# Optimization experiments

Measured on AMD Instinct MI355X. Metric: run time of the kernel, lower is better.

## Reference

```python
import jax, jax.numpy as jnp
import numpy as np

K_EDE = 10.0   # self.k
T_EDE = 0.1    # self.t
BN_EPS = 1e-5
T_A = 576.0    # 3*3*64, hardcoded in my_bn1/my_bn2


def qfn(x, prec):
    # dorefa-style round quantizer with straight-through gradient
    n = float(2 ** prec - 1)
    return x + jax.lax.stop_gradient(jnp.round(x * n) / n - x)


@jax.custom_vjp
def binary_quantize(x):
    return jnp.sign(x)


def _bq_fwd(x):
    return jnp.sign(x), x


def _bq_bwd(x, g):
    # IR-Net EDE backward: k * t * (1 - tanh(x*t)^2)
    return (K_EDE * T_EDE * (1.0 - jnp.tanh(x * T_EDE) ** 2) * g,)


binary_quantize.defvjp(_bq_fwd, _bq_bwd)


def _clip_T(x):
    T = jnp.maximum(jnp.abs(x.min()), jnp.abs(x.max()))
    return jax.lax.stop_gradient(jnp.clip(T, 1e-10, 255.0))


def quantize_conv_act(x, prec):
    # my_quantize_conv: clamp to [-T, T], scale to [-1,1], qfn (no rescale by T)
    T = _clip_T(x)
    return qfn(jnp.clip(x, -T, T) / T, prec)


def quantize(x, prec):
    # my_quantize: same but rescaled back by T
    T = _clip_T(x)
    return qfn(jnp.clip(x, -T, T) / T, prec) * T


def ir_conv2d(a, w, stride):
    # IR-Net 1w8a IRConv2d: per-out-channel normalize, binarize (sign), power-of-2 scale
    co = w.shape[0]
    wf = w.reshape(co, -1)
    bw = (w - wf.mean(1)[:, None, None, None]) / jnp.std(wf, axis=1, ddof=1)[:, None, None, None]
    sw = jax.lax.stop_gradient(
        2.0 ** jnp.round(jnp.log2(jnp.abs(bw.reshape(co, -1)).mean(1)))
    )[:, None, None, None]
    bw = binary_quantize(bw) * sw
    return jax.lax.conv_general_dilated(
        a, bw, window_strides=(stride, stride), padding=[(1, 1), (1, 1)],
        dimension_numbers=('NCHW', 'OIHW', 'NCHW'))


def bn_as_quantized_affine(x, gamma, beta, mean, var):
    # my_bn1/my_bn2 (eval mode): BN folded into per-channel scale+bias.
    # The original builds a CxC diagonal 1x1 conv; since off-diagonal entries are 0,
    # both the quantization stats (max|.|) and the conv reduce exactly to this
    # per-channel affine, which is the faithful fused form.
    std = jnp.sqrt(var + BN_EPS)
    w = gamma / std
    b = beta - w * mean
    qw = quantize(w, 3)
    qb = quantize(b, 12)
    aq = qfn(x / T_A, 10) * T_A  # my_quantize_activation(input, 10, T_a)
    return aq * qw[None, :, None, None] + qb[None, :, None, None]


def _block(x, w1, w2, g1, b1, m1, v1, g2, b2, m2, v2):
    xq = quantize_conv_act(x, 3)
    out = ir_conv2d(xq, w1, 1)
    out = bn_as_quantized_affine(out, g1, b1, m1, v1) + xq  # identity shortcut
    out = jnp.clip(out, -1.0, 1.0)  # hardtanh
    x1 = quantize_conv_act(out, 3)
    out = ir_conv2d(x1, w2, 1)
    out = bn_as_quantized_affine(out, g2, b2, m2, v2) + x1
    return jnp.clip(out, -1.0, 1.0)


def setup_inputs() -> dict:
    key = jax.random.key(0)
    ks = jax.random.split(key, 11)
    B, C, H, W = 128, 64, 56, 56
    return {
        'x': jax.random.normal(ks[0], (B, C, H, W), jnp.float32),
        'w1': jax.random.normal(ks[1], (C, C, 3, 3), jnp.float32) * 0.1,
        'w2': jax.random.normal(ks[2], (C, C, 3, 3), jnp.float32) * 0.1,
        'g1': jax.random.uniform(ks[3], (C,), jnp.float32, 0.5, 1.5),
        'b1': jax.random.normal(ks[4], (C,), jnp.float32) * 0.1,
        'm1': jax.random.normal(ks[5], (C,), jnp.float32) * 0.1,
        'v1': jax.random.uniform(ks[6], (C,), jnp.float32, 0.5, 1.5),
        'g2': jax.random.uniform(ks[7], (C,), jnp.float32, 0.5, 1.5),
        'b2': jax.random.normal(ks[8], (C,), jnp.float32) * 0.1,
        'm2': jax.random.normal(ks[9], (C,), jnp.float32) * 0.1,
        'v2': jax.random.uniform(ks[10], (C,), jnp.float32, 0.5, 1.5),
    }


def reference(x, w1, w2, g1, b1, m1, v1, g2, b2, m2, v2):
    return _block(x, w1, w2, g1, b1, m1, v1, g2, b2, m2, v2)
```

## Files before the change

### kernel.cpp

```cpp
#include <hip/hip_runtime.h>
#include <stdint.h>

typedef int v4i   __attribute__((ext_vector_type(4)));
typedef int v16i  __attribute__((ext_vector_type(16)));

#define B_    128
#define C_    64
#define H_    56
#define W_    56
#define HW_   3136
#define NELEM (B_*C_*HW_)

#define OFF_K0   0
#define OFF_K1   ((size_t)NELEM)
#define OFF_WB   ((size_t)2*NELEM)
#define OFF_PAR  (OFF_WB + 2*9*64*64)
#define OFF_MAX  (OFF_PAR + 384*4)

__global__ void k_absmax(const float* __restrict__ x, unsigned* __restrict__ maxbits) {
    __shared__ float smax[4];
    float m = 0.f;
    const int n4 = NELEM / 4;
    for (int i = blockIdx.x * blockDim.x + threadIdx.x; i < n4; i += gridDim.x * blockDim.x) {
        float4 v = ((const float4*)x)[i];
        m = fmaxf(m, fmaxf(fmaxf(fabsf(v.x), fabsf(v.y)), fmaxf(fabsf(v.z), fabsf(v.w))));
    }
    for (int off = 32; off; off >>= 1) m = fmaxf(m, __shfl_down(m, off, 64));
    if ((threadIdx.x & 63) == 0) smax[threadIdx.x >> 6] = m;
    __syncthreads();
    if (threadIdx.x == 0) {
        float mm = fmaxf(fmaxf(smax[0], smax[1]), fmaxf(smax[2], smax[3]));
        atomicMax(maxbits, __float_as_uint(mm));
    }
}

__global__ void k_quant(const float* __restrict__ x, const unsigned* __restrict__ maxbits,
                        int8_t* __restrict__ k8) {
    __shared__ __align__(16) int8_t tile[W_ * C_];
    const int n = blockIdx.x / H_;
    const int y = blockIdx.x % H_;
    const float T = fminf(fmaxf(__uint_as_float(*maxbits), 1e-10f), 255.0f);
    for (int i = threadIdx.x; i < C_ * 14; i += blockDim.x) {
        int c = i / 14, j = i % 14;
        float4 v = *(const float4*)(x + ((size_t)(n * C_ + c)) * HW_ + y * W_ + j * 4);
        float vv[4] = {v.x, v.y, v.z, v.w};
#pragma unroll
        for (int q = 0; q < 4; q++) {
            float t = fminf(fmaxf(vv[q], -T), T);
            float u = __fdiv_rn(t, T);
            int k = (int)rintf(__fmul_rn(u, 7.0f));
            tile[(j * 4 + q) * C_ + c] = (int8_t)k;
        }
    }
    __syncthreads();
    int4* dst = (int4*)(k8 + ((size_t)(n * H_ + y)) * W_ * C_);
    for (int i = threadIdx.x; i < W_ * C_ / 16; i += blockDim.x)
        dst[i] = ((const int4*)tile)[i];
}

__device__ __forceinline__ float pw_reduce64(float r) {
    r = __fadd_rn(r, __shfl_xor(r, 1, 64));
    r = __fadd_rn(r, __shfl_xor(r, 2, 64));
    r = __fadd_rn(r, __shfl_xor(r, 4, 64));
    r = __fadd_rn(r, __shfl_xor(r, 8, 64));
    r = __fadd_rn(r, __shfl_xor(r, 16, 64));
    r = __fadd_rn(r, __shfl_xor(r, 32, 64));
    return r;
}

__global__ void k_prepw(const float* __restrict__ w1, const float* __restrict__ w2,
                        int8_t* __restrict__ wb, float* __restrict__ par) {
    const int layer = blockIdx.x >> 6;
    const int co    = blockIdx.x & 63;
    const float* w = (layer ? w2 : w1) + (size_t)co * 576;
    const int lane = threadIdx.x;
    const int base = (lane >> 3) * 72 + (lane & 7);

    float v[9];
#pragma unroll
    for (int i = 0; i < 9; i++) v[i] = w[base + 8 * i];

    float s = v[0];
#pragma unroll
    for (int i = 1; i < 9; i++) s = __fadd_rn(s, v[i]);
    const float mean = __fdiv_rn(pw_reduce64(s), 576.0f);

    float d0 = __fsub_rn(v[0], mean);
    float sq = __fmul_rn(d0, d0);
#pragma unroll
    for (int i = 1; i < 9; i++) {
        float d = __fsub_rn(v[i], mean);
        sq = __fadd_rn(sq, __fmul_rn(d, d));
    }
    const float sig = __fsqrt_rn(__fdiv_rn(pw_reduce64(sq), 575.0f));

    float sa = fabsf(__fdiv_rn(__fsub_rn(v[0], mean), sig));
#pragma unroll
    for (int i = 1; i < 9; i++)
        sa = __fadd_rn(sa, fabsf(__fdiv_rn(__fsub_rn(v[i], mean), sig)));
    const float ma = __fdiv_rn(pw_reduce64(sa), 576.0f);
    const float p  = rintf(log2f(ma));
    if (lane == 0) par[256 + layer * 64 + co] = __fdiv_rn(exp2f(p), 7.0f);

#pragma unroll
    for (int i = 0; i < 9; i++) {
        int ig = base + 8 * i;
        float d = __fsub_rn(v[i], mean);
        int8_t sg = (d > 0.0f) ? (int8_t)1 : ((d < 0.0f) ? (int8_t)-1 : (int8_t)0);
        int ci = ig / 9, t = ig % 9;
        wb[(((size_t)layer * 9 + t) * 64 + co) * 64 + ci] = sg;
    }
}

__global__ void k_prepbn(const float* g1, const float* bb1, const float* mm1, const float* vv1,
                         const float* g2, const float* bb2, const float* mm2, const float* vv2,
                         float* __restrict__ par) {
    const int layer = threadIdx.x >> 6;
    const int c = threadIdx.x & 63;
    const float* g  = layer ? g2  : g1;
    const float* be = layer ? bb2 : bb1;
    const float* mu = layer ? mm2 : mm1;
    const float* va = layer ? vv2 : vv1;
    const float stdv = __fsqrt_rn(__fadd_rn(va[c], 1e-5f));
    const float w = __fdiv_rn(g[c], stdv);
    const float b = __fsub_rn(be[c], __fmul_rn(w, mu[c]));
    float aw = fabsf(w), ab = fabsf(b);
    for (int off = 32; off; off >>= 1) {
        aw = fmaxf(aw, __shfl_xor(aw, off, 64));
        ab = fmaxf(ab, __shfl_xor(ab, off, 64));
    }
    const float Tw = fminf(fmaxf(aw, 1e-10f), 255.0f);
    const float Tb = fminf(fmaxf(ab, 1e-10f), 255.0f);
    {
        float vq = __fdiv_rn(fminf(fmaxf(w, -Tw), Tw), Tw);
        float r  = rintf(__fmul_rn(vq, 7.0f));
        float qf = __fadd_rn(vq, __fsub_rn(__fdiv_rn(r, 7.0f), vq));
        par[layer * 64 + c] = __fmul_rn(qf, Tw);
    }
    {
        float vq = __fdiv_rn(fminf(fmaxf(b, -Tb), Tb), Tb);
        float r  = rintf(__fmul_rn(vq, 4095.0f));
        float qf = __fadd_rn(vq, __fsub_rn(__fdiv_rn(r, 4095.0f), vq));
        par[128 + layer * 64 + c] = __fmul_rn(qf, Tb);
    }
}

template <int LAYER>
__global__ __launch_bounds__(256) void k_conv(const int8_t* __restrict__ kin,
                                              const int8_t* __restrict__ wb,
                                              const float* __restrict__ par,
                                              int8_t* __restrict__ kout,
                                              float* __restrict__ fout) {
    __shared__ __align__(16) int8_t halo[4 * 58 * 64];
    __shared__ __align__(16) int8_t wsm[9 * 64 * 64];
    const int n  = blockIdx.x / 28;
    const int y0 = (blockIdx.x % 28) * 2;
    const int tid = threadIdx.x;

    for (int u = tid; u < 928; u += 256) {
        int r = u / 232, rem = u % 232;
        int cp = rem / 4, part = rem % 4;
        int y = y0 - 1 + r, xg = cp - 1;
        int4 val = {0, 0, 0, 0};
        if (y >= 0 && y < 56 && xg >= 0 && xg < 56)
            val = *(const int4*)(kin + (((size_t)(n * 56 + y)) * 56 + xg) * 64 + part * 16);
        *(int4*)(halo + u * 16) = val;
    }
    const int8_t* wsrc = wb + (size_t)(LAYER - 1) * 9 * 64 * 64;
    for (int u = tid; u < 2304; u += 256)
        *(int4*)(wsm + u * 16) = *(const int4*)(wsrc + u * 16);
    __syncthreads();

    const int wv = tid >> 6, lane = tid & 63;
    const int mbase = wv * 32;
    const int ml = lane & 31;
    const int khalf = lane >> 5;
    const int m = mbase + ml;
    const int m_eff = (m < 112) ? m : 111;
    const int rm = m_eff / 56, cm = m_eff % 56;

    v16i acc0, acc1;
#pragma unroll
    for (int i = 0; i < 16; i++) { acc0[i] = 0; acc1[i] = 0; }

#pragma unroll
    for (int s = 0; s < 9; s++) {
        const int ky = s / 3, kx = s % 3;
        const int abase  = ((rm + ky) * 58 + (cm + kx)) * 64 + khalf * 16;
        const int bbase0 = (s * 64 + ml) * 64 + khalf * 16;
        const int bbase1 = (s * 64 + 32 + ml) * 64 + khalf * 16;
#pragma unroll
        for (int kb = 0; kb < 2; kb++) {
            v4i a  = *(const v4i*)(halo + abase  + kb * 32);
            v4i b0 = *(const v4i*)(wsm  + bbase0 + kb * 32);
            v4i b1 = *(const v4i*)(wsm  + bbase1 + kb * 32);
            acc0 = __builtin_amdgcn_mfma_i32_32x32x32_i8(a, b0, acc0, 0, 0, 0);
            acc1 = __builtin_amdgcn_mfma_i32_32x32x32_i8(a, b1, acc1, 0, 0, 0);
        }
    }
    __syncthreads();

    const float* qw = par + (LAYER - 1) * 64;
    const float* qb = par + 128 + (LAYER - 1) * 64;
    const float* sc = par + 256 + (LAYER - 1) * 64;
#pragma unroll
    for (int t = 0; t < 2; t++) {
        const int co = ml + t * 32;
        const float qwf = qw[co], qbf = qb[co], scf = sc[co];
#pragma unroll
        for (int r = 0; r < 16; r++) {
            const int mrow = mbase + (r & 3) + 8 * (r >> 2) + 4 * khalf;
            if (mrow >= 112) continue;
            const float Sf = (float)(t ? acc1[r] : acc0[r]);
            float convf = __fmul_rn(Sf, scf);
            float xb = __fdiv_rn(convf, 576.0f);
            float rr = rintf(__fmul_rn(xb, 1023.0f));
            float q1 = __fdiv_rn(rr, 1023.0f);
            float y1 = __fadd_rn(xb, __fsub_rn(q1, xb));
            float aq = __fmul_rn(y1, 576.0f);
            const int rloc = mrow / 56, cloc = mrow % 56;
            float kcf = (float)halo[((rloc + 1) * 58 + (cloc + 1)) * 64 + co];
            float xqv = __fdiv_rn(kcf, 7.0f);
            float val = __fadd_rn(__fadd_rn(__fmul_rn(aq, qwf), qbf), xqv);
            val = fminf(fmaxf(val, -1.0f), 1.0f);
            if (LAYER == 1) {
                int k2 = (int)rintf(__fmul_rn(val, 7.0f));
                wsm[mrow * 64 + co] = (int8_t)k2;
            } else {
                *(float*)&wsm[((size_t)co * 112 + mrow) * 4] = val;
            }
        }
    }
    __syncthreads();

    const size_t posbase = (size_t)n * HW_ + (size_t)y0 * 56;
    if (LAYER == 1) {
        int4* dst = (int4*)(kout + posbase * 64);
        for (int u = tid; u < 448; u += 256) dst[u] = ((const int4*)wsm)[u];
    } else {
        for (int u = tid; u < 1792; u += 256) {
            int co = u / 28, q = u % 28;
            float4 v = *((const float4*)wsm + co * 28 + q);
            *(float4*)(fout + ((size_t)(n * 64 + co)) * HW_ + (size_t)y0 * 56 + q * 4) = v;
        }
    }
}

extern "C" void kernel_launch(void* const* d_in, const int* in_sizes, int n_in,
                              void* d_out, int out_size, void* d_ws, size_t ws_size,
                              hipStream_t stream) {
    const float* x  = (const float*)d_in[0];
    const float* w1 = (const float*)d_in[1];
    const float* w2 = (const float*)d_in[2];
    const float* g1 = (const float*)d_in[3];
    const float* b1 = (const float*)d_in[4];
    const float* m1 = (const float*)d_in[5];
    const float* v1 = (const float*)d_in[6];
    const float* g2 = (const float*)d_in[7];
    const float* b2 = (const float*)d_in[8];
    const float* m2 = (const float*)d_in[9];
    const float* v2 = (const float*)d_in[10];

    char* ws = (char*)d_ws;
    int8_t*  k0  = (int8_t*)(ws + OFF_K0);
    int8_t*  k1  = (int8_t*)(ws + OFF_K1);
    int8_t*  wbp = (int8_t*)(ws + OFF_WB);
    float*   par = (float*)(ws + OFF_PAR);
    unsigned* mx = (unsigned*)(ws + OFF_MAX);

    hipMemsetAsync(mx, 0, 4, stream);
    k_absmax<<<1024, 256, 0, stream>>>(x, mx);
    k_quant<<<B_ * H_, 256, 0, stream>>>(x, mx, k0);
    k_prepw<<<128, 64, 0, stream>>>(w1, w2, wbp, par);
    k_prepbn<<<1, 128, 0, stream>>>(g1, b1, m1, v1, g2, b2, m2, v2, par);
    k_conv<1><<<B_ * 28, 256, 0, stream>>>(k0, wbp, par, k1, nullptr);
    k_conv<2><<<B_ * 28, 256, 0, stream>>>(k1, wbp, par, nullptr, (float*)d_out);
}
```

Baseline: 351.2 us.

## Merge prep kernels, re-layout halo/weights in 16-channel planes, write conv outputs directly

Folds the absmax, weight-binarization and BN-folding kernels into one launch to cut launch overhead. Halo and weight tiles move to a channel-group-major layout with 16-byte rows, meant to reduce LDS bank conflicts in the MFMA operand loads. The conv epilogue drops the shared-memory staging and its barriers and stores straight to global memory, using byte stores for layer 1 and float4 stores for layer 2. k_quant packs four channels per word through a padded tile, divisions become double-precision reciprocal multiplies, and the conv kernel gets launch_bounds(256,3). The double reciprocal trick may differ from __fdiv_rn in rare rounding cases, and the scattered int8 global stores in layer 1 may coalesce poorly.

```diff
diff --git a/kernel.cpp b/kernel.cpp
--- a/kernel.cpp
+++ b/kernel.cpp
@@ -14,49 +14,8 @@
 #define OFF_K0   0
 #define OFF_K1   ((size_t)NELEM)
 #define OFF_WB   ((size_t)2*NELEM)
-#define OFF_PAR  (OFF_WB + 2*9*64*64)
+#define OFF_PAR  (OFF_WB + 2*4*9*64*16)
 #define OFF_MAX  (OFF_PAR + 384*4)
-
-__global__ void k_absmax(const float* __restrict__ x, unsigned* __restrict__ maxbits) {
-    __shared__ float smax[4];
-    float m = 0.f;
-    const int n4 = NELEM / 4;
-    for (int i = blockIdx.x * blockDim.x + threadIdx.x; i < n4; i += gridDim.x * blockDim.x) {
-        float4 v = ((const float4*)x)[i];
-        m = fmaxf(m, fmaxf(fmaxf(fabsf(v.x), fabsf(v.y)), fmaxf(fabsf(v.z), fabsf(v.w))));
-    }
-    for (int off = 32; off; off >>= 1) m = fmaxf(m, __shfl_down(m, off, 64));
-    if ((threadIdx.x & 63) == 0) smax[threadIdx.x >> 6] = m;
-    __syncthreads();
-    if (threadIdx.x == 0) {
-        float mm = fmaxf(fmaxf(smax[0], smax[1]), fmaxf(smax[2], smax[3]));
-        atomicMax(maxbits, __float_as_uint(mm));
-    }
-}
-
-__global__ void k_quant(const float* __restrict__ x, const unsigned* __restrict__ maxbits,
-                        int8_t* __restrict__ k8) {
-    __shared__ __align__(16) int8_t tile[W_ * C_];
-    const int n = blockIdx.x / H_;
-    const int y = blockIdx.x % H_;
-    const float T = fminf(fmaxf(__uint_as_float(*maxbits), 1e-10f), 255.0f);
-    for (int i = threadIdx.x; i < C_ * 14; i += blockDim.x) {
-        int c = i / 14, j = i % 14;
-        float4 v = *(const float4*)(x + ((size_t)(n * C_ + c)) * HW_ + y * W_ + j * 4);
-        float vv[4] = {v.x, v.y, v.z, v.w};
-#pragma unroll
-        for (int q = 0; q < 4; q++) {
-            float t = fminf(fmaxf(vv[q], -T), T);
-            float u = __fdiv_rn(t, T);
-            int k = (int)rintf(__fmul_rn(u, 7.0f));
-            tile[(j * 4 + q) * C_ + c] = (int8_t)k;
-        }
-    }
-    __syncthreads();
-    int4* dst = (int4*)(k8 + ((size_t)(n * H_ + y)) * W_ * C_);
-    for (int i = threadIdx.x; i < W_ * C_ / 16; i += blockDim.x)
-        dst[i] = ((const int4*)tile)[i];
-}
 
 __device__ __forceinline__ float pw_reduce64(float r) {
     r = __fadd_rn(r, __shfl_xor(r, 1, 64));
@@ -68,105 +27,163 @@
     return r;
 }
 
-__global__ void k_prepw(const float* __restrict__ w1, const float* __restrict__ w2,
-                        int8_t* __restrict__ wb, float* __restrict__ par) {
-    const int layer = blockIdx.x >> 6;
-    const int co    = blockIdx.x & 63;
-    const float* w = (layer ? w2 : w1) + (size_t)co * 576;
-    const int lane = threadIdx.x;
-    const int base = (lane >> 3) * 72 + (lane & 7);
-
-    float v[9];
-#pragma unroll
-    for (int i = 0; i < 9; i++) v[i] = w[base + 8 * i];
-
-    float s = v[0];
-#pragma unroll
-    for (int i = 1; i < 9; i++) s = __fadd_rn(s, v[i]);
-    const float mean = __fdiv_rn(pw_reduce64(s), 576.0f);
-
-    float d0 = __fsub_rn(v[0], mean);
-    float sq = __fmul_rn(d0, d0);
-#pragma unroll
-    for (int i = 1; i < 9; i++) {
-        float d = __fsub_rn(v[i], mean);
-        sq = __fadd_rn(sq, __fmul_rn(d, d));
-    }
-    const float sig = __fsqrt_rn(__fdiv_rn(pw_reduce64(sq), 575.0f));
-
-    float sa = fabsf(__fdiv_rn(__fsub_rn(v[0], mean), sig));
-#pragma unroll
-    for (int i = 1; i < 9; i++)
-        sa = __fadd_rn(sa, fabsf(__fdiv_rn(__fsub_rn(v[i], mean), sig)));
-    const float ma = __fdiv_rn(pw_reduce64(sa), 576.0f);
-    const float p  = rintf(log2f(ma));
-    if (lane == 0) par[256 + layer * 64 + co] = __fdiv_rn(exp2f(p), 7.0f);
-
-#pragma unroll
-    for (int i = 0; i < 9; i++) {
-        int ig = base + 8 * i;
-        float d = __fsub_rn(v[i], mean);
-        int8_t sg = (d > 0.0f) ? (int8_t)1 : ((d < 0.0f) ? (int8_t)-1 : (int8_t)0);
-        int ci = ig / 9, t = ig % 9;
-        wb[(((size_t)layer * 9 + t) * 64 + co) * 64 + ci] = sg;
-    }
-}
-
-__global__ void k_prepbn(const float* g1, const float* bb1, const float* mm1, const float* vv1,
-                         const float* g2, const float* bb2, const float* mm2, const float* vv2,
-                         float* __restrict__ par) {
-    const int layer = threadIdx.x >> 6;
-    const int c = threadIdx.x & 63;
-    const float* g  = layer ? g2  : g1;
-    const float* be = layer ? bb2 : bb1;
-    const float* mu = layer ? mm2 : mm1;
-    const float* va = layer ? vv2 : vv1;
-    const float stdv = __fsqrt_rn(__fadd_rn(va[c], 1e-5f));
-    const float w = __fdiv_rn(g[c], stdv);
-    const float b = __fsub_rn(be[c], __fmul_rn(w, mu[c]));
-    float aw = fabsf(w), ab = fabsf(b);
-    for (int off = 32; off; off >>= 1) {
-        aw = fmaxf(aw, __shfl_xor(aw, off, 64));
-        ab = fmaxf(ab, __shfl_xor(ab, off, 64));
-    }
-    const float Tw = fminf(fmaxf(aw, 1e-10f), 255.0f);
-    const float Tb = fminf(fmaxf(ab, 1e-10f), 255.0f);
-    {
-        float vq = __fdiv_rn(fminf(fmaxf(w, -Tw), Tw), Tw);
-        float r  = rintf(__fmul_rn(vq, 7.0f));
-        float qf = __fadd_rn(vq, __fsub_rn(__fdiv_rn(r, 7.0f), vq));
-        par[layer * 64 + c] = __fmul_rn(qf, Tw);
-    }
-    {
-        float vq = __fdiv_rn(fminf(fmaxf(b, -Tb), Tb), Tb);
-        float r  = rintf(__fmul_rn(vq, 4095.0f));
-        float qf = __fadd_rn(vq, __fsub_rn(__fdiv_rn(r, 4095.0f), vq));
-        par[128 + layer * 64 + c] = __fmul_rn(qf, Tb);
-    }
+__global__ void k_pre(const float* __restrict__ x, unsigned* __restrict__ maxbits,
+                      const float* __restrict__ w1, const float* __restrict__ w2,
+                      int8_t* __restrict__ wb, float* __restrict__ par,
+                      const float* __restrict__ g1, const float* __restrict__ bb1,
+                      const float* __restrict__ mm1, const float* __restrict__ vv1,
+                      const float* __restrict__ g2, const float* __restrict__ bb2,
+                      const float* __restrict__ mm2, const float* __restrict__ vv2) {
+    __shared__ float smax[4];
+    const int b = blockIdx.x;
+    const int tid = threadIdx.x;
+    if (b < 1024) {
+        float m = 0.f;
+        const int n4 = NELEM / 4;
+        for (int i = b * 256 + tid; i < n4; i += 1024 * 256) {
+            float4 v = ((const float4*)x)[i];
+            m = fmaxf(m, fmaxf(fmaxf(fabsf(v.x), fabsf(v.y)), fmaxf(fabsf(v.z), fabsf(v.w))));
+        }
+        for (int off = 32; off; off >>= 1) m = fmaxf(m, __shfl_down(m, off, 64));
+        if ((tid & 63) == 0) smax[tid >> 6] = m;
+        __syncthreads();
+        if (tid == 0) {
+            float mm = fmaxf(fmaxf(smax[0], smax[1]), fmaxf(smax[2], smax[3]));
+            atomicMax(maxbits, __float_as_uint(mm));
+        }
+    } else if (b < 1056) {
+        const int idx = (b - 1024) * 4 + (tid >> 6);
+        const int layer = idx >> 6, co = idx & 63;
+        const int lane = tid & 63;
+        const float* w = (layer ? w2 : w1) + (size_t)co * 576;
+        const int base = (lane >> 3) * 72 + (lane & 7);
+
+        float v[9];
+#pragma unroll
+        for (int i = 0; i < 9; i++) v[i] = w[base + 8 * i];
+
+        float s = v[0];
+#pragma unroll
+        for (int i = 1; i < 9; i++) s = __fadd_rn(s, v[i]);
+        const float mean = __fdiv_rn(pw_reduce64(s), 576.0f);
+
+        float d0 = __fsub_rn(v[0], mean);
+        float sq = __fmul_rn(d0, d0);
+#pragma unroll
+        for (int i = 1; i < 9; i++) {
+            float d = __fsub_rn(v[i], mean);
+            sq = __fadd_rn(sq, __fmul_rn(d, d));
+        }
+        const float sig = __fsqrt_rn(__fdiv_rn(pw_reduce64(sq), 575.0f));
+
+        float sa = fabsf(__fdiv_rn(__fsub_rn(v[0], mean), sig));
+#pragma unroll
+        for (int i = 1; i < 9; i++)
+            sa = __fadd_rn(sa, fabsf(__fdiv_rn(__fsub_rn(v[i], mean), sig)));
+        const float ma = __fdiv_rn(pw_reduce64(sa), 576.0f);
+        const float p  = rintf(log2f(ma));
+        if (lane == 0) par[256 + layer * 64 + co] = __fdiv_rn(exp2f(p), 7.0f);
+
+#pragma unroll
+        for (int i = 0; i < 9; i++) {
+            int ig = base + 8 * i;
+            float d = __fsub_rn(v[i], mean);
+            int8_t sg = (d > 0.0f) ? (int8_t)1 : ((d < 0.0f) ? (int8_t)-1 : (int8_t)0);
+            int ci = ig / 9, tp = ig % 9;
+            wb[((((size_t)layer * 4 + (ci >> 4)) * 9 + tp) * 64 + co) * 16 + (ci & 15)] = sg;
+        }
+    } else {
+        if (tid < 128) {
+            const int layer = tid >> 6;
+            const int c = tid & 63;
+            const float* g  = layer ? g2  : g1;
+            const float* be = layer ? bb2 : bb1;
+            const float* mu = layer ? mm2 : mm1;
+            const float* va = layer ? vv2 : vv1;
+            const float stdv = __fsqrt_rn(__fadd_rn(va[c], 1e-5f));
+            const float w = __fdiv_rn(g[c], stdv);
+            const float bb = __fsub_rn(be[c], __fmul_rn(w, mu[c]));
+            float aw = fabsf(w), ab = fabsf(bb);
+            for (int off = 32; off; off >>= 1) {
+                aw = fmaxf(aw, __shfl_xor(aw, off, 64));
+                ab = fmaxf(ab, __shfl_xor(ab, off, 64));
+            }
+            const float Tw = fminf(fmaxf(aw, 1e-10f), 255.0f);
+            const float Tb = fminf(fmaxf(ab, 1e-10f), 255.0f);
+            {
+                float vq = __fdiv_rn(fminf(fmaxf(w, -Tw), Tw), Tw);
+                float r  = rintf(__fmul_rn(vq, 7.0f));
+                float qf = __fadd_rn(vq, __fsub_rn(__fdiv_rn(r, 7.0f), vq));
+                par[layer * 64 + c] = __fmul_rn(qf, Tw);
+            }
+            {
+                float vq = __fdiv_rn(fminf(fmaxf(bb, -Tb), Tb), Tb);
+                float r  = rintf(__fmul_rn(vq, 4095.0f));
+                float qf = __fadd_rn(vq, __fsub_rn(__fdiv_rn(r, 4095.0f), vq));
+                par[128 + layer * 64 + c] = __fmul_rn(qf, Tb);
+            }
+        }
+    }
+}
+
+__global__ void k_quant(const float* __restrict__ x, const unsigned* __restrict__ maxbits,
+                        int8_t* __restrict__ k8) {
+    __shared__ unsigned tile[56 * 17];
+    const int n = blockIdx.x / H_;
+    const int y = blockIdx.x % H_;
+    const float T = fminf(fmaxf(__uint_as_float(*maxbits), 1e-10f), 255.0f);
+    const double dinv = 1.0 / (double)T;
+    const int t = threadIdx.x;
+    if (t < 224) {
+        const int cb = t / 14, xb = t % 14;
+        const float* src = x + ((size_t)(n * 64 + 4 * cb)) * HW_ + y * 56 + 4 * xb;
+        int kq[4][4];
+#pragma unroll
+        for (int i = 0; i < 4; i++) {
+            float4 v = *(const float4*)(src + (size_t)i * HW_);
+            const float e[4] = {v.x, v.y, v.z, v.w};
+#pragma unroll
+            for (int j = 0; j < 4; j++) {
+                const float tc = fminf(fmaxf(e[j], -T), T);
+                const float u  = (float)((double)tc * dinv);
+                kq[i][j] = (int)rintf(__fmul_rn(u, 7.0f));
+            }
+        }
+#pragma unroll
+        for (int j = 0; j < 4; j++) {
+            const unsigned d = (kq[0][j] & 255) | ((kq[1][j] & 255) << 8) |
+                               ((kq[2][j] & 255) << 16) | ((unsigned)(kq[3][j] & 255) << 24);
+            tile[(4 * xb + j) * 17 + cb] = d;
+        }
+    }
+    __syncthreads();
+    unsigned* dst = (unsigned*)(k8 + ((size_t)(n * 56 + y)) * 56 * 64);
+    for (int u = t; u < 896; u += 256)
+        dst[u] = tile[(u >> 4) * 17 + (u & 15)];
 }
 
 template <int LAYER>
-__global__ __launch_bounds__(256) void k_conv(const int8_t* __restrict__ kin,
-                                              const int8_t* __restrict__ wb,
-                                              const float* __restrict__ par,
-                                              int8_t* __restrict__ kout,
-                                              float* __restrict__ fout) {
-    __shared__ __align__(16) int8_t halo[4 * 58 * 64];
-    __shared__ __align__(16) int8_t wsm[9 * 64 * 64];
+__global__ __launch_bounds__(256, 3) void k_conv(const int8_t* __restrict__ kin,
+                                                 const int8_t* __restrict__ wb,
+                                                 const float* __restrict__ par,
+                                                 int8_t* __restrict__ kout,
+                                                 float* __restrict__ fout) {
+    __shared__ __align__(16) int8_t halo[4 * 4 * 58 * 16];
+    __shared__ __align__(16) int8_t wsm[4 * 9 * 64 * 16];
     const int n  = blockIdx.x / 28;
     const int y0 = (blockIdx.x % 28) * 2;
     const int tid = threadIdx.x;
 
     for (int u = tid; u < 928; u += 256) {
-        int r = u / 232, rem = u % 232;
-        int cp = rem / 4, part = rem % 4;
-        int y = y0 - 1 + r, xg = cp - 1;
+        const int q = u & 3, v = u >> 2;
+        const int r = v / 58, xp = v % 58;
+        const int y = y0 - 1 + r, xg = xp - 1;
         int4 val = {0, 0, 0, 0};
         if (y >= 0 && y < 56 && xg >= 0 && xg < 56)
-            val = *(const int4*)(kin + (((size_t)(n * 56 + y)) * 56 + xg) * 64 + part * 16);
-        *(int4*)(halo + u * 16) = val;
-    }
-    const int8_t* wsrc = wb + (size_t)(LAYER - 1) * 9 * 64 * 64;
+            val = *(const int4*)(kin + (((size_t)(n * 56 + y)) * 56 + xg) * 64 + q * 16);
+        *(int4*)(halo + (((q * 4 + r) * 58 + xp) << 4)) = val;
+    }
+    const int8_t* wsrc = wb + (size_t)(LAYER - 1) * (4 * 9 * 64 * 16);
     for (int u = tid; u < 2304; u += 256)
         *(int4*)(wsm + u * 16) = *(const int4*)(wsrc + u * 16);
     __syncthreads();
@@ -186,19 +203,16 @@
 #pragma unroll
     for (int s = 0; s < 9; s++) {
         const int ky = s / 3, kx = s % 3;
-        const int abase  = ((rm + ky) * 58 + (cm + kx)) * 64 + khalf * 16;
-        const int bbase0 = (s * 64 + ml) * 64 + khalf * 16;
-        const int bbase1 = (s * 64 + 32 + ml) * 64 + khalf * 16;
 #pragma unroll
         for (int kb = 0; kb < 2; kb++) {
-            v4i a  = *(const v4i*)(halo + abase  + kb * 32);
-            v4i b0 = *(const v4i*)(wsm  + bbase0 + kb * 32);
-            v4i b1 = *(const v4i*)(wsm  + bbase1 + kb * 32);
+            const int q = khalf + 2 * kb;
+            v4i a  = *(const v4i*)(halo + ((((q * 4 + rm + ky) * 58) + cm + kx) << 4));
+            v4i b0 = *(const v4i*)(wsm  + (((q * 9 + s) * 64 + ml) << 4));
+            v4i b1 = *(const v4i*)(wsm  + (((q * 9 + s) * 64 + 32 + ml) << 4));
             acc0 = __builtin_amdgcn_mfma_i32_32x32x32_i8(a, b0, acc0, 0, 0, 0);
             acc1 = __builtin_amdgcn_mfma_i32_32x32x32_i8(a, b1, acc1, 0, 0, 0);
         }
     }
-    __syncthreads();
 
     const float* qw = par + (LAYER - 1) * 64;
     const float* qb = par + 128 + (LAYER - 1) * 64;
@@ -207,41 +221,40 @@
     for (int t = 0; t < 2; t++) {
         const int co = ml + t * 32;
         const float qwf = qw[co], qbf = qb[co], scf = sc[co];
-#pragma unroll
-        for (int r = 0; r < 16; r++) {
-            const int mrow = mbase + (r & 3) + 8 * (r >> 2) + 4 * khalf;
-            if (mrow >= 112) continue;
-            const float Sf = (float)(t ? acc1[r] : acc0[r]);
-            float convf = __fmul_rn(Sf, scf);
-            float xb = __fdiv_rn(convf, 576.0f);
-            float rr = rintf(__fmul_rn(xb, 1023.0f));
-            float q1 = __fdiv_rn(rr, 1023.0f);
-            float y1 = __fadd_rn(xb, __fsub_rn(q1, xb));
-            float aq = __fmul_rn(y1, 576.0f);
-            const int rloc = mrow / 56, cloc = mrow % 56;
-            float kcf = (float)halo[((rloc + 1) * 58 + (cloc + 1)) * 64 + co];
-            float xqv = __fdiv_rn(kcf, 7.0f);
-            float val = __fadd_rn(__fadd_rn(__fmul_rn(aq, qwf), qbf), xqv);
-            val = fminf(fmaxf(val, -1.0f), 1.0f);
-            if (LAYER == 1) {
-                int k2 = (int)rintf(__fmul_rn(val, 7.0f));
-                wsm[mrow * 64 + co] = (int8_t)k2;
-            } else {
-                *(float*)&wsm[((size_t)co * 112 + mrow) * 4] = val;
-            }
-        }
-    }
-    __syncthreads();
-
-    const size_t posbase = (size_t)n * HW_ + (size_t)y0 * 56;
-    if (LAYER == 1) {
-        int4* dst = (int4*)(kout + posbase * 64);
-        for (int u = tid; u < 448; u += 256) dst[u] = ((const int4*)wsm)[u];
-    } else {
-        for (int u = tid; u < 1792; u += 256) {
-            int co = u / 28, q = u % 28;
-            float4 v = *((const float4*)wsm + co * 28 + q);
-            *(float4*)(fout + ((size_t)(n * 64 + co)) * HW_ + (size_t)y0 * 56 + q * 4) = v;
+        const int qc = co >> 4, cl = co & 15;
+#pragma unroll
+        for (int g = 0; g < 4; g++) {
+            const int mb = mbase + 8 * g + 4 * khalf;
+            if (mb >= 112) continue;
+            const int rloc = (mb >= 56) ? 1 : 0;
+            const int cl0  = mb - 56 * rloc;
+            const int hb   = (((qc * 4 + rloc + 1) * 58) + cl0 + 1) * 16 + cl;
+            float vals[4];
+#pragma unroll
+            for (int i = 0; i < 4; i++) {
+                const int   S  = t ? acc1[4 * g + i] : acc0[4 * g + i];
+                const float Sf = (float)S;
+                const float convf = __fmul_rn(Sf, scf);
+                const float xb = (float)((double)convf * (1.0 / 576.0));
+                const float rr = rintf(__fmul_rn(xb, 1023.0f));
+                const float q1 = (float)((double)rr * (1.0 / 1023.0));
+                const float y1 = __fadd_rn(xb, __fsub_rn(q1, xb));
+                const float aq = __fmul_rn(y1, 576.0f);
+                const int   kc = (int)halo[hb + 16 * i];
+                const float xqv = (float)((double)kc * (1.0 / 7.0));
+                float val = __fadd_rn(__fadd_rn(__fmul_rn(aq, qwf), qbf), xqv);
+                val = fminf(fmaxf(val, -1.0f), 1.0f);
+                if (LAYER == 1) {
+                    const int k2 = (int)rintf(__fmul_rn(val, 7.0f));
+                    kout[(((size_t)(n * 56 + y0 + rloc)) * 56 + cl0 + i) * 64 + co] = (int8_t)k2;
+                } else {
+                    vals[i] = val;
+                }
+            }
+            if (LAYER == 2) {
+                float4 o = make_float4(vals[0], vals[1], vals[2], vals[3]);
+                *(float4*)(fout + ((size_t)(n * 64 + co)) * HW_ + y0 * 56 + mb) = o;
+            }
         }
     }
 }
@@ -269,10 +282,9 @@
     unsigned* mx = (unsigned*)(ws + OFF_MAX);
 
     hipMemsetAsync(mx, 0, 4, stream);
-    k_absmax<<<1024, 256, 0, stream>>>(x, mx);
+    k_pre<<<1057, 256, 0, stream>>>(x, mx, w1, w2, wbp, par,
+                                    g1, b1, m1, v1, g2, b2, m2, v2);
     k_quant<<<B_ * H_, 256, 0, stream>>>(x, mx, k0);
-    k_prepw<<<128, 64, 0, stream>>>(w1, w2, wbp, par);
-    k_prepbn<<<1, 128, 0, stream>>>(g1, b1, m1, v1, g2, b2, m2, v2, par);
     k_conv<1><<<B_ * 28, 256, 0, stream>>>(k0, wbp, par, k1, nullptr);
     k_conv<2><<<B_ * 28, 256, 0, stream>>>(k1, wbp, par, nullptr, (float*)d_out);
 }
```

Result: faster. 321.7 us (-8.4%).
